# Kernel optimization log

Measured on AMD Instinct MI355X. Metric: run time of the kernel, lower is better.

Reference implementation:

```python
import jax, jax.numpy as jnp
import numpy as np

N_NODES = 30000
N_EDGES = 480000
NODE_DIM = 16
NUM_RADIAL = 8
NUM_ELEMENTS = 120
R_MAX = 5.0
NUM_BLOCKS = 2
N_PATHS = 5  # h0*sh0->0e, h0*sh1->1o, h0*sh2->2e, h1.sh1->0e, h2.sh2->0e


def _sh_basis(u):
    # real spherical harmonics up to l=2, component normalization, on unit vectors u [E,3]
    x, y, z = u[:, 0], u[:, 1], u[:, 2]
    s15 = jnp.sqrt(jnp.asarray(15.0, u.dtype))
    s5 = jnp.sqrt(jnp.asarray(5.0, u.dtype))
    sh1 = jnp.sqrt(jnp.asarray(3.0, u.dtype)) * u                      # [E,3]
    sh2 = jnp.stack([s15 * x * y, s15 * y * z,
                     0.5 * s5 * (3.0 * z * z - 1.0),
                     s15 * x * z, 0.5 * s15 * (x * x - y * y)], -1)    # [E,5]
    return sh1, sh2


def _energy(pos, emb, W_init, Wr, br, W_out, W_read, W1, b1, W2, b2, z, edge_index):
    N = pos.shape[0]
    row, col = edge_index[0], edge_index[1]
    edge_vec = pos[row] - pos[col]                                     # [E,3] gather
    r = jnp.sqrt(jnp.sum(edge_vec * edge_vec, -1) + 1e-12)             # [E]
    n = jnp.arange(1, NUM_RADIAL + 1, dtype=pos.dtype)
    # Bessel radial basis: sqrt(2/rc) * sin(n*pi*r/rc)/r
    radial = jnp.sqrt(2.0 / R_MAX) * jnp.sin(n[None, :] * jnp.pi * r[:, None] / R_MAX) / r[:, None]  # [E,R]
    u = edge_vec / r[:, None]
    sh1, sh2 = _sh_basis(u)

    # initial projection: embedding scalars -> 0e channels; l=1,l=2 start at zero
    h0 = emb[z] @ W_init                                               # [N,C]
    h1 = jnp.zeros((N, NODE_DIM, 3), pos.dtype)
    h2 = jnp.zeros((N, NODE_DIM, 5), pos.dtype)

    for b in range(NUM_BLOCKS):
        w = (radial @ Wr[b] + br[b]).reshape(-1, N_PATHS, NODE_DIM)    # [E,P,C] radial path weights
        h0c, h1c, h2c = h0[col], h1[col], h2[col]
        # scalar messages: h0*sh0 + <h1,sh1> + <h2,sh2>
        m0 = (w[:, 0] * h0c
              + w[:, 3] * jnp.einsum('ecm,em->ec', h1c, sh1)
              + w[:, 4] * jnp.einsum('ecm,em->ec', h2c, sh2))          # [E,C]
        m1 = (w[:, 1] * h0c)[:, :, None] * sh1[:, None, :]             # [E,C,3]
        m2 = (w[:, 2] * h0c)[:, :, None] * sh2[:, None, :]             # [E,C,5]
        a0 = jax.ops.segment_sum(m0, row, num_segments=N)
        a1 = jax.ops.segment_sum(m1, row, num_segments=N)
        a2 = jax.ops.segment_sum(m2, row, num_segments=N)
        h0 = h0 + a0 @ W_out[b, 0]
        h1 = h1 + jnp.einsum('ncm,cd->ndm', a1, W_out[b, 1])
        h2 = h2 + jnp.einsum('ncm,cd->ndm', a2, W_out[b, 2])

    inv = h0 @ W_read                                                  # readout 0e part
    site = jax.nn.silu(inv @ W1 + b1) @ W2 + b2                        # [N,1]
    return jnp.sum(site)


def setup_inputs() -> dict:
    key = jax.random.key(0)
    ks = jax.random.split(key, 12)
    C, R = NODE_DIM, NUM_RADIAL
    s = 1.0 / np.sqrt(C)
    return {
        'pos': jax.random.normal(ks[0], (N_NODES, 3), jnp.float32) * 3.0,
        'z': jax.random.randint(ks[1], (N_NODES,), 0, NUM_ELEMENTS),
        'edge_index': jax.random.randint(ks[2], (2, N_EDGES), 0, N_NODES),
        'emb': jax.random.normal(ks[3], (NUM_ELEMENTS, C), jnp.float32),
        'W_init': jax.random.normal(ks[4], (C, C), jnp.float32) * s,
        'Wr': jax.random.normal(ks[5], (NUM_BLOCKS, R, N_PATHS * C), jnp.float32) / np.sqrt(R),
        'br': jnp.zeros((NUM_BLOCKS, N_PATHS * C), jnp.float32),
        'W_out': jax.random.normal(ks[6], (NUM_BLOCKS, 3, C, C), jnp.float32) * s,
        'W_read': jax.random.normal(ks[7], (C, C), jnp.float32) * s,
        'W1': jax.random.normal(ks[8], (C, C), jnp.float32) * s,
        'b1': jnp.zeros((C,), jnp.float32),
        'W2': jax.random.normal(ks[9], (C, 1), jnp.float32) * s,
        'b2': jnp.zeros((1,), jnp.float32),
    }


def reference(pos, z, edge_index, emb, W_init, Wr, br, W_out, W_read, W1, b1, W2, b2):
    e_fn = lambda p: _energy(p, emb, W_init, Wr, br, W_out, W_read, W1, b1, W2, b2, z, edge_index)
    total, dE_dpos = jax.value_and_grad(e_fn)(pos)
    energy = jnp.reshape(total, (1, 1))
    forces = -dE_dpos
    return energy, forces
```

## Files before the change

kernel.cpp:

```cpp
#include <hip/hip_runtime.h>
#include <math.h>

#ifndef M_PI
#define M_PI 3.14159265358979323846
#endif

static inline int cdiv(int a, int b){ return (a + b - 1) / b; }

#define SQRT3f  1.7320508075688772f
#define SQRT5f  2.23606797749979f
#define SQRT15f 3.872983346207417f
#define KRADf   0.6324555320336759f
#define PI5f    0.6283185307179586f

__device__ __forceinline__ float grp16_sum(float v){
  v += __shfl_xor(v, 1, 64);
  v += __shfl_xor(v, 2, 64);
  v += __shfl_xor(v, 4, 64);
  v += __shfl_xor(v, 8, 64);
  return v;
}
__device__ __forceinline__ float xgrp_sum(float v){
  v += __shfl_xor(v, 16, 64);
  v += __shfl_xor(v, 32, 64);
  return v;
}

__device__ __forceinline__ void sh_from_u(float ux, float uy, float uz,
                                          float* sh1, float* sh2)
{
  sh1[0] = SQRT3f*ux; sh1[1] = SQRT3f*uy; sh1[2] = SQRT3f*uz;
  sh2[0] = SQRT15f*ux*uy;
  sh2[1] = SQRT15f*uy*uz;
  sh2[2] = 0.5f*SQRT5f*(3.f*uz*uz - 1.f);
  sh2[3] = SQRT15f*ux*uz;
  sh2[4] = 0.5f*SQRT15f*(ux*ux - uy*uy);
}

__global__ void k_hist(const int* __restrict__ ei, int E,
                       int* __restrict__ deg_row, int* __restrict__ deg_col)
{
  int e = blockIdx.x * blockDim.x + threadIdx.x;
  if (e >= E) return;
  atomicAdd(&deg_row[ei[e]], 1);
  atomicAdd(&deg_col[ei[E + e]], 1);
}

__global__ void k_alloc(const int* __restrict__ deg_row, const int* __restrict__ deg_col,
                        int* __restrict__ start_row, int* __restrict__ cur_row,
                        int* __restrict__ start_col, int* __restrict__ cur_col,
                        int* __restrict__ cursors, int N)
{
  int idx = blockIdx.x * blockDim.x + threadIdx.x;
  int lane = threadIdx.x & 63;
  #pragma unroll
  for (int which = 0; which < 2; which++) {
    const int* deg = which ? deg_col : deg_row;
    int* start = which ? start_col : start_row;
    int* cur   = which ? cur_col   : cur_row;
    int v = (idx < N) ? deg[idx] : 0;
    int incl = v;
    #pragma unroll
    for (int d = 1; d < 64; d <<= 1) {
      int y = __shfl_up(incl, d, 64);
      if (lane >= d) incl += y;
    }
    int wtot = __shfl(incl, 63, 64);
    int base = 0;
    if (lane == 63) base = atomicAdd(&cursors[which], wtot);
    base = __shfl(base, 63, 64);
    if (idx < N) { int st = base + incl - v; start[idx] = st; cur[idx] = st; }
  }
}

__global__ void k_scatter_geom(const float* __restrict__ pos, const int* __restrict__ ei, int E,
                               int* __restrict__ cur_row, int* __restrict__ cur_col,
                               float4* __restrict__ geoR,
                               int* __restrict__ colR, int* __restrict__ cposR,
                               int* __restrict__ rowC, int* __restrict__ rposC)
{
  int e = blockIdx.x * blockDim.x + threadIdx.x;
  if (e >= E) return;
  int row = ei[e], col = ei[E + e];
  int pr = atomicAdd(&cur_row[row], 1);
  int pc = atomicAdd(&cur_col[col], 1);
  colR[pr] = col; cposR[pr] = pc;
  rowC[pc] = row; rposC[pc] = pr;

  float px = pos[row*3+0] - pos[col*3+0];
  float py = pos[row*3+1] - pos[col*3+1];
  float pz = pos[row*3+2] - pos[col*3+2];
  float r2 = px*px + py*py + pz*pz + 1e-12f;
  float r = sqrtf(r2);
  float inv_r = 1.0f / r;
  float ux = px*inv_r, uy = py*inv_r, uz = pz*inv_r;
  float x = r * PI5f;
  float s1, c1;
  sincosf(x, &s1, &c1);
  float tc = 2.f * c1;
  float sprev = 0.f, s = s1, cprev = 1.f, cc = c1;
  float Ki = KRADf * inv_r;
  float rad[8], draddr[8];
  const float KPI5 = KRADf * PI5f;
  #pragma unroll
  for (int k = 0; k < 8; k++) {
    rad[k] = Ki * s;
    draddr[k] = (KPI5 * (float)(k+1) * cc - rad[k]) * inv_r;
    float sn = tc*s - sprev; sprev = s; s = sn;
    float cn = tc*cc - cprev; cprev = cc; cc = cn;
  }
  geoR[pr*5+0] = make_float4(rad[0], rad[1], rad[2], rad[3]);
  geoR[pr*5+1] = make_float4(rad[4], rad[5], rad[6], rad[7]);
  geoR[pr*5+2] = make_float4(draddr[0], draddr[1], draddr[2], draddr[3]);
  geoR[pr*5+3] = make_float4(draddr[4], draddr[5], draddr[6], draddr[7]);
  geoR[pr*5+4] = make_float4(ux, uy, uz, inv_r);
}

__global__ void k_node_init(const float* __restrict__ emb, const int* __restrict__ z,
                            const float* __restrict__ W_init, float* __restrict__ h0, int N)
{
  __shared__ float sW[256];
  if (threadIdx.x < 256) sW[threadIdx.x] = W_init[threadIdx.x];
  __syncthreads();
  int n = blockIdx.x * blockDim.x + threadIdx.x;
  if (n >= N) return;
  const float* e = emb + z[n]*16;
  float ev[16];
  #pragma unroll
  for (int k = 0; k < 16; k++) ev[k] = e[k];
  #pragma unroll
  for (int c = 0; c < 16; c++) {
    float s = 0.f;
    #pragma unroll
    for (int k = 0; k < 16; k++) s += ev[k] * sW[k*16+c];
    h0[n*16+c] = s;
  }
}

__global__ void k_fwd_b0(const float* __restrict__ Wr, const float* __restrict__ br,
                         const float* __restrict__ h0_in, const float4* __restrict__ geoR,
                         const int* __restrict__ colR,
                         const int* __restrict__ start_row, const int* __restrict__ deg_row,
                         float* __restrict__ a0, float* __restrict__ a1, float* __restrict__ a2,
                         int N)
{
  int n = (blockIdx.x * blockDim.x + threadIdx.x) >> 6;
  int lane = threadIdx.x & 63;
  int g = lane >> 4, c = lane & 15;
  if (n >= N) return;
  float wr0[8], wr1[8], wr2[8];
  #pragma unroll
  for (int k = 0; k < 8; k++) {
    wr0[k] = Wr[k*80 + c];
    wr1[k] = Wr[k*80 + 16 + c];
    wr2[k] = Wr[k*80 + 32 + c];
  }
  float b0v = br[c], b1v = br[16 + c], b2v = br[32 + c];

  float acc0 = 0.f, acc1[3] = {0.f,0.f,0.f}, acc2[5] = {0.f,0.f,0.f,0.f,0.f};

  int i0 = start_row[n] + g, i1 = start_row[n] + deg_row[n];
  float4 G0n = {0,0,0,0}, G1n = {0,0,0,0}, G4n = {0,0,0,0};
  float h0n = 0.f;
  if (i0 < i1) {
    G0n = geoR[i0*5+0]; G1n = geoR[i0*5+1]; G4n = geoR[i0*5+4];
    h0n = h0_in[colR[i0]*16 + c];
  }
  for (int i = i0; i < i1; i += 4) {
    float4 G0 = G0n, G1 = G1n, G4 = G4n;
    float h0c = h0n;
    if (i+4 < i1) {
      G0n = geoR[(i+4)*5+0]; G1n = geoR[(i+4)*5+1]; G4n = geoR[(i+4)*5+4];
      h0n = h0_in[colR[i+4]*16 + c];
    }
    float rad[8] = {G0.x,G0.y,G0.z,G0.w,G1.x,G1.y,G1.z,G1.w};
    float sh1[3], sh2[5];
    sh_from_u(G4.x, G4.y, G4.z, sh1, sh2);
    float w0 = b0v, w1 = b1v, w2 = b2v;
    #pragma unroll
    for (int k = 0; k < 8; k++) {
      w0 += rad[k]*wr0[k]; w1 += rad[k]*wr1[k]; w2 += rad[k]*wr2[k];
    }
    acc0 += w0*h0c;
    float wh1 = w1*h0c, wh2 = w2*h0c;
    #pragma unroll
    for (int m = 0; m < 3; m++) acc1[m] += wh1*sh1[m];
    #pragma unroll
    for (int m = 0; m < 5; m++) acc2[m] += wh2*sh2[m];
  }
  acc0 = xgrp_sum(acc0);
  #pragma unroll
  for (int m = 0; m < 3; m++) acc1[m] = xgrp_sum(acc1[m]);
  #pragma unroll
  for (int m = 0; m < 5; m++) acc2[m] = xgrp_sum(acc2[m]);
  if (g == 0) {
    a0[n*16 + c] = acc0;
    #pragma unroll
    for (int m = 0; m < 3; m++) a1[n*48 + c*3 + m] = acc1[m];
    #pragma unroll
    for (int m = 0; m < 5; m++) a2[n*80 + c*5 + m] = acc2[m];
  }
}

__global__ void k_fwd_b1(const float* __restrict__ Wr, const float* __restrict__ br,
                         const float* __restrict__ h0_in, const float* __restrict__ h1_in,
                         const float* __restrict__ h2_in, const float4* __restrict__ geoR,
                         const int* __restrict__ colR,
                         const int* __restrict__ start_row, const int* __restrict__ deg_row,
                         float* __restrict__ a0, int N)
{
  int n = (blockIdx.x * blockDim.x + threadIdx.x) >> 6;
  int lane = threadIdx.x & 63;
  int g = lane >> 4, c = lane & 15;
  if (n >= N) return;
  float wr0[8], wr3[8], wr4[8];
  #pragma unroll
  for (int k = 0; k < 8; k++) {
    wr0[k] = Wr[k*80 + c];
    wr3[k] = Wr[k*80 + 48 + c];
    wr4[k] = Wr[k*80 + 64 + c];
  }
  float b0v = br[c], b3v = br[48 + c], b4v = br[64 + c];

  float acc0 = 0.f;
  int i0 = start_row[n] + g, i1 = start_row[n] + deg_row[n];
  float4 G0n = {0,0,0,0}, G1n = {0,0,0,0}, G4n = {0,0,0,0};
  float h0n = 0.f, h1n[3] = {0,0,0}, h2n[5] = {0,0,0,0,0};
  if (i0 < i1) {
    int col = colR[i0];
    G0n = geoR[i0*5+0]; G1n = geoR[i0*5+1]; G4n = geoR[i0*5+4];
    h0n = h0_in[col*16 + c];
    #pragma unroll
    for (int m = 0; m < 3; m++) h1n[m] = h1_in[col*48 + c*3 + m];
    #pragma unroll
    for (int m = 0; m < 5; m++) h2n[m] = h2_in[col*80 + c*5 + m];
  }
  for (int i = i0; i < i1; i += 4) {
    float4 G0 = G0n, G1 = G1n, G4 = G4n;
    float h0c = h0n;
    float h1c[3], h2c[5];
    #pragma unroll
    for (int m = 0; m < 3; m++) h1c[m] = h1n[m];
    #pragma unroll
    for (int m = 0; m < 5; m++) h2c[m] = h2n[m];
    if (i+4 < i1) {
      int col = colR[i+4];
      G0n = geoR[(i+4)*5+0]; G1n = geoR[(i+4)*5+1]; G4n = geoR[(i+4)*5+4];
      h0n = h0_in[col*16 + c];
      #pragma unroll
      for (int m = 0; m < 3; m++) h1n[m] = h1_in[col*48 + c*3 + m];
      #pragma unroll
      for (int m = 0; m < 5; m++) h2n[m] = h2_in[col*80 + c*5 + m];
    }
    float rad[8] = {G0.x,G0.y,G0.z,G0.w,G1.x,G1.y,G1.z,G1.w};
    float sh1[3], sh2[5];
    sh_from_u(G4.x, G4.y, G4.z, sh1, sh2);
    float w0 = b0v, w3 = b3v, w4 = b4v;
    #pragma unroll
    for (int k = 0; k < 8; k++) {
      w0 += rad[k]*wr0[k]; w3 += rad[k]*wr3[k]; w4 += rad[k]*wr4[k];
    }
    float S1 = 0.f, S2 = 0.f;
    #pragma unroll
    for (int m = 0; m < 3; m++) S1 += h1c[m]*sh1[m];
    #pragma unroll
    for (int m = 0; m < 5; m++) S2 += h2c[m]*sh2[m];
    acc0 += w0*h0c + w3*S1 + w4*S2;
  }
  acc0 = xgrp_sum(acc0);
  if (g == 0) a0[n*16 + c] = acc0;
}

__global__ void k_node_update(const float* __restrict__ h0_in,
                              const float* __restrict__ a0, const float* __restrict__ a1,
                              const float* __restrict__ a2,
                              const float* __restrict__ U,
                              float* __restrict__ h0_out, float* __restrict__ h1_out,
                              float* __restrict__ h2_out, int N, int full)
{
  int idx = blockIdx.x * blockDim.x + threadIdx.x;
  int n = idx >> 4, d = idx & 15;
  if (n >= N) return;
  const float* U0 = U;
  const float* U1 = U + 256;
  const float* U2 = U + 512;
  float s = h0_in[n*16 + d];
  #pragma unroll
  for (int c = 0; c < 16; c++) s += a0[n*16 + c] * U0[c*16 + d];
  h0_out[n*16 + d] = s;
  if (full) {
    float v1[3] = {0.f, 0.f, 0.f};
    #pragma unroll
    for (int c = 0; c < 16; c++) {
      float u = U1[c*16 + d];
      #pragma unroll
      for (int m = 0; m < 3; m++) v1[m] += a1[n*48 + c*3 + m] * u;
    }
    #pragma unroll
    for (int m = 0; m < 3; m++) h1_out[n*48 + d*3 + m] = v1[m];
    float v2[5] = {0.f, 0.f, 0.f, 0.f, 0.f};
    #pragma unroll
    for (int c = 0; c < 16; c++) {
      float u = U2[c*16 + d];
      #pragma unroll
      for (int m = 0; m < 5; m++) v2[m] += a2[n*80 + c*5 + m] * u;
    }
    #pragma unroll
    for (int m = 0; m < 5; m++) h2_out[n*80 + d*5 + m] = v2[m];
  }
}

__global__ void k_readout_bwd(const float* __restrict__ h0, const float* __restrict__ W_read,
                              const float* __restrict__ W1, const float* __restrict__ b1,
                              const float* __restrict__ W2, const float* __restrict__ b2,
                              const float* __restrict__ U0b1,
                              float* __restrict__ g0, float* __restrict__ ga0,
                              float* __restrict__ energy, int N)
{
  int n = blockIdx.x * blockDim.x + threadIdx.x;
  float site = 0.f;
  if (n < N) {
    float h[16], inv[16], dt[16], g0v[16];
    #pragma unroll
    for (int d = 0; d < 16; d++) h[d] = h0[n*16 + d];
    #pragma unroll
    for (int j = 0; j < 16; j++) {
      float s = 0.f;
      #pragma unroll
      for (int d = 0; d < 16; d++) s += h[d] * W_read[d*16 + j];
      inv[j] = s;
    }
    site = b2[0];
    #pragma unroll
    for (int c = 0; c < 16; c++) {
      float t = b1[c];
      #pragma unroll
      for (int j = 0; j < 16; j++) t += inv[j] * W1[j*16 + c];
      float sg = 1.f / (1.f + expf(-t));
      float w2v = W2[c];
      site += t * sg * w2v;
      dt[c] = w2v * sg * (1.f + t * (1.f - sg));
    }
    float dinv[16];
    #pragma unroll
    for (int j = 0; j < 16; j++) {
      float s = 0.f;
      #pragma unroll
      for (int c = 0; c < 16; c++) s += dt[c] * W1[j*16 + c];
      dinv[j] = s;
    }
    #pragma unroll
    for (int d = 0; d < 16; d++) {
      float s = 0.f;
      #pragma unroll
      for (int j = 0; j < 16; j++) s += dinv[j] * W_read[d*16 + j];
      g0v[d] = s;
      g0[n*16 + d] = s;
    }
    #pragma unroll
    for (int c = 0; c < 16; c++) {
      float s = 0.f;
      #pragma unroll
      for (int d = 0; d < 16; d++) s += g0v[d] * U0b1[c*16 + d];
      ga0[n*16 + c] = s;
    }
  }
  #pragma unroll
  for (int off = 32; off; off >>= 1) site += __shfl_down(site, off, 64);
  if ((threadIdx.x & 63) == 0) atomicAdd(energy, site);
}

__global__ void k_ga(const float* __restrict__ g0, const float* __restrict__ g1,
                     const float* __restrict__ g2, const float* __restrict__ U,
                     float* __restrict__ ga0, float* __restrict__ ga1, float* __restrict__ ga2,
                     int N)
{
  int idx = blockIdx.x * blockDim.x + threadIdx.x;
  int n = idx >> 4, c = idx & 15;
  if (n >= N) return;
  const float* U0 = U;
  const float* U1 = U + 256;
  const float* U2 = U + 512;
  float s = 0.f;
  #pragma unroll
  for (int d = 0; d < 16; d++) s += g0[n*16 + d] * U0[c*16 + d];
  ga0[n*16 + c] = s;
  float v1[3] = {0.f, 0.f, 0.f};
  #pragma unroll
  for (int d = 0; d < 16; d++) {
    float u = U1[c*16 + d];
    #pragma unroll
    for (int m = 0; m < 3; m++) v1[m] += g1[n*48 + d*3 + m] * u;
  }
  #pragma unroll
  for (int m = 0; m < 3; m++) ga1[n*48 + c*3 + m] = v1[m];
  float v2[5] = {0.f, 0.f, 0.f, 0.f, 0.f};
  #pragma unroll
  for (int d = 0; d < 16; d++) {
    float u = U2[c*16 + d];
    #pragma unroll
    for (int m = 0; m < 5; m++) v2[m] += g2[n*80 + d*5 + m] * u;
  }
  #pragma unroll
  for (int m = 0; m < 5; m++) ga2[n*80 + c*5 + m] = v2[m];
}

__global__ void k_bwd_b1_col(const float* __restrict__ Wr, const float* __restrict__ br,
                             const float* __restrict__ h0_in, const float* __restrict__ h1_in,
                             const float* __restrict__ h2_in,
                             const float* __restrict__ ga0, const float4* __restrict__ geoR,
                             const int* __restrict__ rowC, const int* __restrict__ rposC,
                             const int* __restrict__ start_col, const int* __restrict__ deg_col,
                             float* __restrict__ g0, float* __restrict__ g1, float* __restrict__ g2,
                             float* __restrict__ dv_col, int N)
{
  int n = (blockIdx.x * blockDim.x + threadIdx.x) >> 6;
  int lane = threadIdx.x & 63;
  int g = lane >> 4, c = lane & 15;
  if (n >= N) return;
  float wr0[8], wr3[8], wr4[8];
  #pragma unroll
  for (int k = 0; k < 8; k++) {
    wr0[k] = Wr[k*80 + c];
    wr3[k] = Wr[k*80 + 48 + c];
    wr4[k] = Wr[k*80 + 64 + c];
  }
  float b0v = br[c], b3v = br[48 + c], b4v = br[64 + c];

  float h0c = h0_in[n*16 + c];
  float h1c[3], h2c[5];
  #pragma unroll
  for (int m = 0; m < 3; m++) h1c[m] = h1_in[n*48 + c*3 + m];
  #pragma unroll
  for (int m = 0; m < 5; m++) h2c[m] = h2_in[n*80 + c*5 + m];

  float accg0 = 0.f, accg1[3] = {0.f,0.f,0.f}, accg2[5] = {0.f,0.f,0.f,0.f,0.f};

  int i0 = start_col[n] + g, i1 = start_col[n] + deg_col[n];
  float4 G0n = {0,0,0,0}, G1n = {0,0,0,0}, G2n = {0,0,0,0}, G3n = {0,0,0,0}, G4n = {0,0,0,0};
  float dm0n = 0.f;
  if (i0 < i1) {
    int rp = rposC[i0];
    G0n = geoR[rp*5+0]; G1n = geoR[rp*5+1]; G2n = geoR[rp*5+2];
    G3n = geoR[rp*5+3]; G4n = geoR[rp*5+4];
    dm0n = ga0[rowC[i0]*16 + c];
  }
  for (int i = i0; i < i1; i += 4) {
    float4 G0 = G0n, G1 = G1n, G2 = G2n, G3 = G3n, G4 = G4n;
    float dm0 = dm0n;
    if (i+4 < i1) {
      int rp = rposC[i+4];
      G0n = geoR[rp*5+0]; G1n = geoR[rp*5+1]; G2n = geoR[rp*5+2];
      G3n = geoR[rp*5+3]; G4n = geoR[rp*5+4];
      dm0n = ga0[rowC[i+4]*16 + c];
    }
    float rad[8]    = {G0.x,G0.y,G0.z,G0.w,G1.x,G1.y,G1.z,G1.w};
    float draddr[8] = {G2.x,G2.y,G2.z,G2.w,G3.x,G3.y,G3.z,G3.w};
    float ux = G4.x, uy = G4.y, uz = G4.z, inv_r = G4.w;
    float sh1[3], sh2[5];
    sh_from_u(ux, uy, uz, sh1, sh2);

    float w0 = b0v, w3 = b3v, w4 = b4v;
    #pragma unroll
    for (int k = 0; k < 8; k++) {
      w0 += rad[k]*wr0[k]; w3 += rad[k]*wr3[k]; w4 += rad[k]*wr4[k];
    }

    float S1 = 0.f, S2 = 0.f;
    #pragma unroll
    for (int m = 0; m < 3; m++) S1 += h1c[m]*sh1[m];
    #pragma unroll
    for (int m = 0; m < 5; m++) S2 += h2c[m]*sh2[m];

    float dw0 = dm0 * h0c;
    float dw3 = dm0 * S1;
    float dw4 = dm0 * S2;
    float t3 = dm0 * w3, t4 = dm0 * w4;

    accg0 += dm0 * w0;
    #pragma unroll
    for (int m = 0; m < 3; m++) accg1[m] += t3 * sh1[m];
    #pragma unroll
    for (int m = 0; m < 5; m++) accg2[m] += t4 * sh2[m];

    float q1x = t3*h1c[0], q1y = t3*h1c[1], q1z = t3*h1c[2];
    float q0 = t4*h2c[0], q1 = t4*h2c[1], q2 = t4*h2c[2], q3 = t4*h2c[3], q4 = t4*h2c[4];
    float gr = 0.f;
    #pragma unroll
    for (int k = 0; k < 8; k++)
      gr += (dw0*wr0[k] + dw3*wr3[k] + dw4*wr4[k]) * draddr[k];
    float gux = SQRT3f*q1x + SQRT15f*(uy*q0 + uz*q3 + ux*q4);
    float guy = SQRT3f*q1y + SQRT15f*(ux*q0 + uz*q1 - uy*q4);
    float guz = SQRT3f*q1z + SQRT15f*uy*q1 + 3.f*SQRT5f*uz*q2 + SQRT15f*ux*q3;

    gr  = grp16_sum(gr);
    gux = grp16_sum(gux);
    guy = grp16_sum(guy);
    guz = grp16_sum(guz);

    if (c == 0) {
      float gdotu = gux*ux + guy*uy + guz*uz;
      dv_col[i*3+0] = gr*ux + (gux - gdotu*ux)*inv_r;
      dv_col[i*3+1] = gr*uy + (guy - gdotu*uy)*inv_r;
      dv_col[i*3+2] = gr*uz + (guz - gdotu*uz)*inv_r;
    }
  }
  accg0 = xgrp_sum(accg0);
  #pragma unroll
  for (int m = 0; m < 3; m++) accg1[m] = xgrp_sum(accg1[m]);
  #pragma unroll
  for (int m = 0; m < 5; m++) accg2[m] = xgrp_sum(accg2[m]);
  if (g == 0) {
    g0[n*16 + c] += accg0;
    #pragma unroll
    for (int m = 0; m < 3; m++) g1[n*48 + c*3 + m] = accg1[m];
    #pragma unroll
    for (int m = 0; m < 5; m++) g2[n*80 + c*5 + m] = accg2[m];
  }
}

__global__ void k_bwd_b0_row(const float* __restrict__ Wr, const float* __restrict__ br,
                             const float* __restrict__ h0_in,
                             const float* __restrict__ ga0, const float* __restrict__ ga1,
                             const float* __restrict__ ga2, const float4* __restrict__ geoR,
                             const int* __restrict__ colR, const int* __restrict__ cposR,
                             const int* __restrict__ start_row, const int* __restrict__ deg_row,
                             float* __restrict__ dv_col, int N)
{
  int n = (blockIdx.x * blockDim.x + threadIdx.x) >> 6;
  int lane = threadIdx.x & 63;
  int g = lane >> 4, c = lane & 15;
  if (n >= N) return;
  float wr0[8], wr1[8], wr2[8];
  #pragma unroll
  for (int k = 0; k < 8; k++) {
    wr0[k] = Wr[k*80 + c];
    wr1[k] = Wr[k*80 + 16 + c];
    wr2[k] = Wr[k*80 + 32 + c];
  }
  float b1v = br[16 + c], b2v = br[32 + c];

  float dm0 = ga0[n*16 + c];
  float dm1[3], dm2[5];
  #pragma unroll
  for (int m = 0; m < 3; m++) dm1[m] = ga1[n*48 + c*3 + m];
  #pragma unroll
  for (int m = 0; m < 5; m++) dm2[m] = ga2[n*80 + c*5 + m];

  int i0 = start_row[n] + g, i1 = start_row[n] + deg_row[n];
  float4 G0n = {0,0,0,0}, G1n = {0,0,0,0}, G2n = {0,0,0,0}, G3n = {0,0,0,0}, G4n = {0,0,0,0};
  float h0n = 0.f;
  if (i0 < i1) {
    G0n = geoR[i0*5+0]; G1n = geoR[i0*5+1]; G2n = geoR[i0*5+2];
    G3n = geoR[i0*5+3]; G4n = geoR[i0*5+4];
    h0n = h0_in[colR[i0]*16 + c];
  }
  for (int i = i0; i < i1; i += 4) {
    float4 G0 = G0n, G1 = G1n, G2 = G2n, G3 = G3n, G4 = G4n;
    float h0c = h0n;
    if (i+4 < i1) {
      G0n = geoR[(i+4)*5+0]; G1n = geoR[(i+4)*5+1]; G2n = geoR[(i+4)*5+2];
      G3n = geoR[(i+4)*5+3]; G4n = geoR[(i+4)*5+4];
      h0n = h0_in[colR[i+4]*16 + c];
    }
    float rad[8]    = {G0.x,G0.y,G0.z,G0.w,G1.x,G1.y,G1.z,G1.w};
    float draddr[8] = {G2.x,G2.y,G2.z,G2.w,G3.x,G3.y,G3.z,G3.w};
    float ux = G4.x, uy = G4.y, uz = G4.z, inv_r = G4.w;
    float sh1[3], sh2[5];
    sh_from_u(ux, uy, uz, sh1, sh2);

    float w1 = b1v, w2v = b2v;
    #pragma unroll
    for (int k = 0; k < 8; k++) { w1 += rad[k]*wr1[k]; w2v += rad[k]*wr2[k]; }

    float T1 = 0.f, T2 = 0.f;
    #pragma unroll
    for (int m = 0; m < 3; m++) T1 += dm1[m]*sh1[m];
    #pragma unroll
    for (int m = 0; m < 5; m++) T2 += dm2[m]*sh2[m];

    float dw0 = dm0 * h0c;
    float dw1 = h0c * T1;
    float dw2 = h0c * T2;

    float w1h = w1*h0c, w2h = w2v*h0c;
    float q1x = dm1[0]*w1h, q1y = dm1[1]*w1h, q1z = dm1[2]*w1h;
    float q0 = dm2[0]*w2h, q1 = dm2[1]*w2h, q2 = dm2[2]*w2h, q3 = dm2[3]*w2h, q4 = dm2[4]*w2h;

    float gr = 0.f;
    #pragma unroll
    for (int k = 0; k < 8; k++)
      gr += (dw0*wr0[k] + dw1*wr1[k] + dw2*wr2[k]) * draddr[k];
    float gux = SQRT3f*q1x + SQRT15f*(uy*q0 + uz*q3 + ux*q4);
    float guy = SQRT3f*q1y + SQRT15f*(ux*q0 + uz*q1 - uy*q4);
    float guz = SQRT3f*q1z + SQRT15f*uy*q1 + 3.f*SQRT5f*uz*q2 + SQRT15f*ux*q3;

    gr  = grp16_sum(gr);
    gux = grp16_sum(gux);
    guy = grp16_sum(guy);
    guz = grp16_sum(guz);

    if (c == 0) {
      int cp = cposR[i];
      float gdotu = gux*ux + guy*uy + guz*uz;
      dv_col[cp*3+0] += gr*ux + (gux - gdotu*ux)*inv_r;
      dv_col[cp*3+1] += gr*uy + (guy - gdotu*uy)*inv_r;
      dv_col[cp*3+2] += gr*uz + (guz - gdotu*uz)*inv_r;
    }
  }
}

__global__ void k_force(const int* __restrict__ start_row, const int* __restrict__ deg_row,
                        const int* __restrict__ cposR,
                        const int* __restrict__ start_col, const int* __restrict__ deg_col,
                        const float* __restrict__ dv_col, float* __restrict__ force, int N)
{
  int n = blockIdx.x * blockDim.x + threadIdx.x;
  if (n >= N) return;
  float fx = 0.f, fy = 0.f, fz = 0.f;
  int c0 = start_col[n], c1 = c0 + deg_col[n];
  for (int i = c0; i < c1; i++) {
    fx += dv_col[i*3+0]; fy += dv_col[i*3+1]; fz += dv_col[i*3+2];
  }
  int r0 = start_row[n], r1 = r0 + deg_row[n];
  for (int i = r0; i < r1; i++) {
    int cp = cposR[i];
    fx -= dv_col[cp*3+0]; fy -= dv_col[cp*3+1]; fz -= dv_col[cp*3+2];
  }
  force[n*3+0] = fx; force[n*3+1] = fy; force[n*3+2] = fz;
}

extern "C" void kernel_launch(void* const* d_in, const int* in_sizes, int n_in,
                              void* d_out, int out_size, void* d_ws, size_t ws_size,
                              hipStream_t stream)
{
  const float* pos    = (const float*)d_in[0];
  const int*   z      = (const int*)  d_in[1];
  const int*   ei     = (const int*)  d_in[2];
  const float* emb    = (const float*)d_in[3];
  const float* W_init = (const float*)d_in[4];
  const float* Wr     = (const float*)d_in[5];
  const float* br     = (const float*)d_in[6];
  const float* W_out  = (const float*)d_in[7];
  const float* W_read = (const float*)d_in[8];
  const float* W1     = (const float*)d_in[9];
  const float* b1     = (const float*)d_in[10];
  const float* W2     = (const float*)d_in[11];
  const float* b2     = (const float*)d_in[12];

  const int N = in_sizes[0] / 3;
  const int E = in_sizes[2] / 2;

  float* f = (float*)d_ws;
  float* geo_f = f; f += (size_t)E*20;
  float* h0_s0 = f; f += (size_t)N*16;
  float* h0_s1 = f; f += (size_t)N*16;
  float* h0_s2 = f; f += (size_t)N*16;
  float* h1_s1 = f; f += (size_t)N*48;
  float* h2_s1 = f; f += (size_t)N*80;
  float* a0    = f; f += (size_t)N*16;
  float* a1    = f; f += (size_t)N*48;
  float* a2    = f; f += (size_t)N*80;
  float* g0    = f; f += (size_t)N*16;
  float* g1    = f; f += (size_t)N*48;
  float* g2    = f; f += (size_t)N*80;
  float* dv    = f; f += (size_t)E*3;
  int* ip = (int*)f;
  int* cursors   = ip; ip += 2;
  int* deg_row   = ip; ip += N;
  int* deg_col   = ip; ip += N;
  int* start_row = ip; ip += N;
  int* start_col = ip; ip += N;
  int* cur_row   = ip; ip += N;
  int* cur_col   = ip; ip += N;
  int* colR      = ip; ip += E;
  int* cposR     = ip; ip += E;
  int* rowC      = ip; ip += E;
  int* rposC     = ip; ip += E;

  float4* geoR = (float4*)geo_f;

  float* out    = (float*)d_out;
  float* energy = out;
  float* force  = out + 1;

  const int BLK = 256;
  const int NPB = BLK / 64;
  const int GPB = BLK / 16;

  (void)hipMemsetAsync(energy, 0, sizeof(float), stream);
  (void)hipMemsetAsync(cursors, 0, (size_t)(2 + 2*N) * sizeof(int), stream);

  k_hist<<<cdiv(E, BLK), BLK, 0, stream>>>(ei, E, deg_row, deg_col);
  k_alloc<<<cdiv(N, BLK), BLK, 0, stream>>>(deg_row, deg_col, start_row, cur_row,
                                            start_col, cur_col, cursors, N);
  k_scatter_geom<<<cdiv(E, BLK), BLK, 0, stream>>>(pos, ei, E, cur_row, cur_col,
                                                   geoR, colR, cposR, rowC, rposC);

  k_node_init<<<cdiv(N, BLK), BLK, 0, stream>>>(emb, z, W_init, h0_s0, N);

  k_fwd_b0<<<cdiv(N, NPB), BLK, 0, stream>>>(Wr, br, h0_s0, geoR, colR,
                                             start_row, deg_row, a0, a1, a2, N);
  k_node_update<<<cdiv(N*16, BLK), BLK, 0, stream>>>(h0_s0, a0, a1, a2,
                                                     W_out, h0_s1, h1_s1, h2_s1, N, 1);

  k_fwd_b1<<<cdiv(N, NPB), BLK, 0, stream>>>(Wr + 640, br + 80,
                                             h0_s1, h1_s1, h2_s1, geoR, colR,
                                             start_row, deg_row, a0, N);
  k_node_update<<<cdiv(N*16, BLK), BLK, 0, stream>>>(h0_s1, a0, nullptr, nullptr,
                                                     W_out + 768, h0_s2, nullptr, nullptr, N, 0);

  k_readout_bwd<<<cdiv(N, BLK), BLK, 0, stream>>>(h0_s2, W_read, W1, b1, W2, b2,
                                                  W_out + 768, g0, a0, energy, N);

  k_bwd_b1_col<<<cdiv(N, NPB), BLK, 0, stream>>>(Wr + 640, br + 80,
                                                 h0_s1, h1_s1, h2_s1, a0, geoR,
                                                 rowC, rposC, start_col, deg_col,
                                                 g0, g1, g2, dv, N);

  k_ga<<<cdiv(N*16, BLK), BLK, 0, stream>>>(g0, g1, g2, W_out, a0, a1, a2, N);
  k_bwd_b0_row<<<cdiv(N, NPB), BLK, 0, stream>>>(Wr, br, h0_s0,
                                                 a0, a1, a2, geoR, colR, cposR,
                                                 start_row, deg_row, dv, N);

  k_force<<<cdiv(N, BLK), BLK, 0, stream>>>(start_row, deg_row, cposR,
                                            start_col, deg_col, dv, force, N);
}
```

Measured before the change: 529.3 us.

## Store compact edge geometry in row and col order, recompute radial basis on the fly

Replaces the 80-byte per-edge geometry record (radial, radial derivative, unit vector) with a 16-byte unit vector plus an 8-byte sin/cos pair, duplicated in row-sorted and col-sorted order. Each edge kernel now rebuilds the Bessel radial values and their derivatives from sin/cos with the Chebyshev recurrence. The col-ordered backward kernel reads contiguous data instead of gathering through rposC. The row backward kernel writes its own dv buffer directly, removing a read-modify-write via cposR, and the force kernel combines both buffers. This trades memory traffic and indirect gathers for a little extra ALU work and one extra E*3 buffer.

```diff
diff --git a/kernel.cpp b/kernel.cpp
--- a/kernel.cpp
+++ b/kernel.cpp
@@ -37,6 +37,33 @@
   sh2[4] = 0.5f*SQRT15f*(ux*ux - uy*uy);
 }
 
+__device__ __forceinline__ void rad_from_sc(float s1, float c1, float inv_r, float* rad)
+{
+  float tc = 2.f * c1;
+  float sprev = 0.f, s = s1;
+  float Ki = KRADf * inv_r;
+  #pragma unroll
+  for (int k = 0; k < 8; k++) {
+    rad[k] = Ki * s;
+    float sn = tc*s - sprev; sprev = s; s = sn;
+  }
+}
+__device__ __forceinline__ void rad_drad_from_sc(float s1, float c1, float inv_r,
+                                                 float* rad, float* draddr)
+{
+  float tc = 2.f * c1;
+  float sprev = 0.f, s = s1, cprev = 1.f, cc = c1;
+  float Ki = KRADf * inv_r;
+  const float KPI5 = KRADf * PI5f;
+  #pragma unroll
+  for (int k = 0; k < 8; k++) {
+    rad[k] = Ki * s;
+    draddr[k] = (KPI5 * (float)(k+1) * cc - rad[k]) * inv_r;
+    float sn = tc*s - sprev; sprev = s; s = sn;
+    float cn = tc*cc - cprev; cprev = cc; cc = cn;
+  }
+}
+
 __global__ void k_hist(const int* __restrict__ ei, int E,
                        int* __restrict__ deg_row, int* __restrict__ deg_col)
 {
@@ -75,7 +102,8 @@
 
 __global__ void k_scatter_geom(const float* __restrict__ pos, const int* __restrict__ ei, int E,
                                int* __restrict__ cur_row, int* __restrict__ cur_col,
-                               float4* __restrict__ geoR,
+                               float4* __restrict__ uR, float2* __restrict__ scR,
+                               float4* __restrict__ uC, float2* __restrict__ scC,
                                int* __restrict__ colR, int* __restrict__ cposR,
                                int* __restrict__ rowC, int* __restrict__ rposC)
 {
@@ -94,26 +122,12 @@
   float r = sqrtf(r2);
   float inv_r = 1.0f / r;
   float ux = px*inv_r, uy = py*inv_r, uz = pz*inv_r;
-  float x = r * PI5f;
   float s1, c1;
-  sincosf(x, &s1, &c1);
-  float tc = 2.f * c1;
-  float sprev = 0.f, s = s1, cprev = 1.f, cc = c1;
-  float Ki = KRADf * inv_r;
-  float rad[8], draddr[8];
-  const float KPI5 = KRADf * PI5f;
-  #pragma unroll
-  for (int k = 0; k < 8; k++) {
-    rad[k] = Ki * s;
-    draddr[k] = (KPI5 * (float)(k+1) * cc - rad[k]) * inv_r;
-    float sn = tc*s - sprev; sprev = s; s = sn;
-    float cn = tc*cc - cprev; cprev = cc; cc = cn;
-  }
-  geoR[pr*5+0] = make_float4(rad[0], rad[1], rad[2], rad[3]);
-  geoR[pr*5+1] = make_float4(rad[4], rad[5], rad[6], rad[7]);
-  geoR[pr*5+2] = make_float4(draddr[0], draddr[1], draddr[2], draddr[3]);
-  geoR[pr*5+3] = make_float4(draddr[4], draddr[5], draddr[6], draddr[7]);
-  geoR[pr*5+4] = make_float4(ux, uy, uz, inv_r);
+  sincosf(r * PI5f, &s1, &c1);
+  float4 u4 = make_float4(ux, uy, uz, inv_r);
+  float2 sc = make_float2(s1, c1);
+  uR[pr] = u4; scR[pr] = sc;
+  uC[pc] = u4; scC[pc] = sc;
 }
 
 __global__ void k_node_init(const float* __restrict__ emb, const int* __restrict__ z,
@@ -138,7 +152,8 @@
 }
 
 __global__ void k_fwd_b0(const float* __restrict__ Wr, const float* __restrict__ br,
-                         const float* __restrict__ h0_in, const float4* __restrict__ geoR,
+                         const float* __restrict__ h0_in,
+                         const float4* __restrict__ uR, const float2* __restrict__ scR,
                          const int* __restrict__ colR,
                          const int* __restrict__ start_row, const int* __restrict__ deg_row,
                          float* __restrict__ a0, float* __restrict__ a1, float* __restrict__ a2,
@@ -160,22 +175,23 @@
   float acc0 = 0.f, acc1[3] = {0.f,0.f,0.f}, acc2[5] = {0.f,0.f,0.f,0.f,0.f};
 
   int i0 = start_row[n] + g, i1 = start_row[n] + deg_row[n];
-  float4 G0n = {0,0,0,0}, G1n = {0,0,0,0}, G4n = {0,0,0,0};
+  float4 Un = {0,0,0,0}; float2 SCn = {0,0};
   float h0n = 0.f;
   if (i0 < i1) {
-    G0n = geoR[i0*5+0]; G1n = geoR[i0*5+1]; G4n = geoR[i0*5+4];
+    Un = uR[i0]; SCn = scR[i0];
     h0n = h0_in[colR[i0]*16 + c];
   }
   for (int i = i0; i < i1; i += 4) {
-    float4 G0 = G0n, G1 = G1n, G4 = G4n;
+    float4 U = Un; float2 SC = SCn;
     float h0c = h0n;
     if (i+4 < i1) {
-      G0n = geoR[(i+4)*5+0]; G1n = geoR[(i+4)*5+1]; G4n = geoR[(i+4)*5+4];
+      Un = uR[i+4]; SCn = scR[i+4];
       h0n = h0_in[colR[i+4]*16 + c];
     }
-    float rad[8] = {G0.x,G0.y,G0.z,G0.w,G1.x,G1.y,G1.z,G1.w};
+    float rad[8];
+    rad_from_sc(SC.x, SC.y, U.w, rad);
     float sh1[3], sh2[5];
-    sh_from_u(G4.x, G4.y, G4.z, sh1, sh2);
+    sh_from_u(U.x, U.y, U.z, sh1, sh2);
     float w0 = b0v, w1 = b1v, w2 = b2v;
     #pragma unroll
     for (int k = 0; k < 8; k++) {
@@ -204,7 +220,8 @@
 
 __global__ void k_fwd_b1(const float* __restrict__ Wr, const float* __restrict__ br,
                          const float* __restrict__ h0_in, const float* __restrict__ h1_in,
-                         const float* __restrict__ h2_in, const float4* __restrict__ geoR,
+                         const float* __restrict__ h2_in,
+                         const float4* __restrict__ uR, const float2* __restrict__ scR,
                          const int* __restrict__ colR,
                          const int* __restrict__ start_row, const int* __restrict__ deg_row,
                          float* __restrict__ a0, int N)
@@ -224,11 +241,11 @@
 
   float acc0 = 0.f;
   int i0 = start_row[n] + g, i1 = start_row[n] + deg_row[n];
-  float4 G0n = {0,0,0,0}, G1n = {0,0,0,0}, G4n = {0,0,0,0};
+  float4 Un = {0,0,0,0}; float2 SCn = {0,0};
   float h0n = 0.f, h1n[3] = {0,0,0}, h2n[5] = {0,0,0,0,0};
   if (i0 < i1) {
     int col = colR[i0];
-    G0n = geoR[i0*5+0]; G1n = geoR[i0*5+1]; G4n = geoR[i0*5+4];
+    Un = uR[i0]; SCn = scR[i0];
     h0n = h0_in[col*16 + c];
     #pragma unroll
     for (int m = 0; m < 3; m++) h1n[m] = h1_in[col*48 + c*3 + m];
@@ -236,7 +253,7 @@
     for (int m = 0; m < 5; m++) h2n[m] = h2_in[col*80 + c*5 + m];
   }
   for (int i = i0; i < i1; i += 4) {
-    float4 G0 = G0n, G1 = G1n, G4 = G4n;
+    float4 U = Un; float2 SC = SCn;
     float h0c = h0n;
     float h1c[3], h2c[5];
     #pragma unroll
@@ -245,16 +262,17 @@
     for (int m = 0; m < 5; m++) h2c[m] = h2n[m];
     if (i+4 < i1) {
       int col = colR[i+4];
-      G0n = geoR[(i+4)*5+0]; G1n = geoR[(i+4)*5+1]; G4n = geoR[(i+4)*5+4];
+      Un = uR[i+4]; SCn = scR[i+4];
       h0n = h0_in[col*16 + c];
       #pragma unroll
       for (int m = 0; m < 3; m++) h1n[m] = h1_in[col*48 + c*3 + m];
       #pragma unroll
       for (int m = 0; m < 5; m++) h2n[m] = h2_in[col*80 + c*5 + m];
     }
-    float rad[8] = {G0.x,G0.y,G0.z,G0.w,G1.x,G1.y,G1.z,G1.w};
+    float rad[8];
+    rad_from_sc(SC.x, SC.y, U.w, rad);
     float sh1[3], sh2[5];
-    sh_from_u(G4.x, G4.y, G4.z, sh1, sh2);
+    sh_from_u(U.x, U.y, U.z, sh1, sh2);
     float w0 = b0v, w3 = b3v, w4 = b4v;
     #pragma unroll
     for (int k = 0; k < 8; k++) {
@@ -408,8 +426,9 @@
 __global__ void k_bwd_b1_col(const float* __restrict__ Wr, const float* __restrict__ br,
                              const float* __restrict__ h0_in, const float* __restrict__ h1_in,
                              const float* __restrict__ h2_in,
-                             const float* __restrict__ ga0, const float4* __restrict__ geoR,
-                             const int* __restrict__ rowC, const int* __restrict__ rposC,
+                             const float* __restrict__ ga0,
+                             const float4* __restrict__ uC, const float2* __restrict__ scC,
+                             const int* __restrict__ rowC,
                              const int* __restrict__ start_col, const int* __restrict__ deg_col,
                              float* __restrict__ g0, float* __restrict__ g1, float* __restrict__ g2,
                              float* __restrict__ dv_col, int N)
@@ -437,26 +456,22 @@
   float accg0 = 0.f, accg1[3] = {0.f,0.f,0.f}, accg2[5] = {0.f,0.f,0.f,0.f,0.f};
 
   int i0 = start_col[n] + g, i1 = start_col[n] + deg_col[n];
-  float4 G0n = {0,0,0,0}, G1n = {0,0,0,0}, G2n = {0,0,0,0}, G3n = {0,0,0,0}, G4n = {0,0,0,0};
+  float4 Un = {0,0,0,0}; float2 SCn = {0,0};
   float dm0n = 0.f;
   if (i0 < i1) {
-    int rp = rposC[i0];
-    G0n = geoR[rp*5+0]; G1n = geoR[rp*5+1]; G2n = geoR[rp*5+2];
-    G3n = geoR[rp*5+3]; G4n = geoR[rp*5+4];
+    Un = uC[i0]; SCn = scC[i0];
     dm0n = ga0[rowC[i0]*16 + c];
   }
   for (int i = i0; i < i1; i += 4) {
-    float4 G0 = G0n, G1 = G1n, G2 = G2n, G3 = G3n, G4 = G4n;
+    float4 U = Un; float2 SC = SCn;
     float dm0 = dm0n;
     if (i+4 < i1) {
-      int rp = rposC[i+4];
-      G0n = geoR[rp*5+0]; G1n = geoR[rp*5+1]; G2n = geoR[rp*5+2];
-      G3n = geoR[rp*5+3]; G4n = geoR[rp*5+4];
+      Un = uC[i+4]; SCn = scC[i+4];
       dm0n = ga0[rowC[i+4]*16 + c];
     }
-    float rad[8]    = {G0.x,G0.y,G0.z,G0.w,G1.x,G1.y,G1.z,G1.w};
-    float draddr[8] = {G2.x,G2.y,G2.z,G2.w,G3.x,G3.y,G3.z,G3.w};
-    float ux = G4.x, uy = G4.y, uz = G4.z, inv_r = G4.w;
+    float rad[8], draddr[8];
+    rad_drad_from_sc(SC.x, SC.y, U.w, rad, draddr);
+    float ux = U.x, uy = U.y, uz = U.z, inv_r = U.w;
     float sh1[3], sh2[5];
     sh_from_u(ux, uy, uz, sh1, sh2);
 
@@ -522,10 +537,11 @@
 __global__ void k_bwd_b0_row(const float* __restrict__ Wr, const float* __restrict__ br,
                              const float* __restrict__ h0_in,
                              const float* __restrict__ ga0, const float* __restrict__ ga1,
-                             const float* __restrict__ ga2, const float4* __restrict__ geoR,
-                             const int* __restrict__ colR, const int* __restrict__ cposR,
+                             const float* __restrict__ ga2,
+                             const float4* __restrict__ uR, const float2* __restrict__ scR,
+                             const int* __restrict__ colR,
                              const int* __restrict__ start_row, const int* __restrict__ deg_row,
-                             float* __restrict__ dv_col, int N)
+                             float* __restrict__ dv_row, int N)
 {
   int n = (blockIdx.x * blockDim.x + threadIdx.x) >> 6;
   int lane = threadIdx.x & 63;
@@ -548,24 +564,22 @@
   for (int m = 0; m < 5; m++) dm2[m] = ga2[n*80 + c*5 + m];
 
   int i0 = start_row[n] + g, i1 = start_row[n] + deg_row[n];
-  float4 G0n = {0,0,0,0}, G1n = {0,0,0,0}, G2n = {0,0,0,0}, G3n = {0,0,0,0}, G4n = {0,0,0,0};
+  float4 Un = {0,0,0,0}; float2 SCn = {0,0};
   float h0n = 0.f;
   if (i0 < i1) {
-    G0n = geoR[i0*5+0]; G1n = geoR[i0*5+1]; G2n = geoR[i0*5+2];
-    G3n = geoR[i0*5+3]; G4n = geoR[i0*5+4];
+    Un = uR[i0]; SCn = scR[i0];
     h0n = h0_in[colR[i0]*16 + c];
   }
   for (int i = i0; i < i1; i += 4) {
-    float4 G0 = G0n, G1 = G1n, G2 = G2n, G3 = G3n, G4 = G4n;
+    float4 U = Un; float2 SC = SCn;
     float h0c = h0n;
     if (i+4 < i1) {
-      G0n = geoR[(i+4)*5+0]; G1n = geoR[(i+4)*5+1]; G2n = geoR[(i+4)*5+2];
-      G3n = geoR[(i+4)*5+3]; G4n = geoR[(i+4)*5+4];
+      Un = uR[i+4]; SCn = scR[i+4];
       h0n = h0_in[colR[i+4]*16 + c];
     }
-    float rad[8]    = {G0.x,G0.y,G0.z,G0.w,G1.x,G1.y,G1.z,G1.w};
-    float draddr[8] = {G2.x,G2.y,G2.z,G2.w,G3.x,G3.y,G3.z,G3.w};
-    float ux = G4.x, uy = G4.y, uz = G4.z, inv_r = G4.w;
+    float rad[8], draddr[8];
+    rad_drad_from_sc(SC.x, SC.y, U.w, rad, draddr);
+    float ux = U.x, uy = U.y, uz = U.z, inv_r = U.w;
     float sh1[3], sh2[5];
     sh_from_u(ux, uy, uz, sh1, sh2);
 
@@ -601,11 +615,10 @@
     guz = grp16_sum(guz);
 
     if (c == 0) {
-      int cp = cposR[i];
       float gdotu = gux*ux + guy*uy + guz*uz;
-      dv_col[cp*3+0] += gr*ux + (gux - gdotu*ux)*inv_r;
-      dv_col[cp*3+1] += gr*uy + (guy - gdotu*uy)*inv_r;
-      dv_col[cp*3+2] += gr*uz + (guz - gdotu*uz)*inv_r;
+      dv_row[i*3+0] = gr*ux + (gux - gdotu*ux)*inv_r;
+      dv_row[i*3+1] = gr*uy + (guy - gdotu*uy)*inv_r;
+      dv_row[i*3+2] = gr*uz + (guz - gdotu*uz)*inv_r;
     }
   }
 }
@@ -613,19 +626,26 @@
 __global__ void k_force(const int* __restrict__ start_row, const int* __restrict__ deg_row,
                         const int* __restrict__ cposR,
                         const int* __restrict__ start_col, const int* __restrict__ deg_col,
-                        const float* __restrict__ dv_col, float* __restrict__ force, int N)
+                        const int* __restrict__ rposC,
+                        const float* __restrict__ dv_col, const float* __restrict__ dv_row,
+                        float* __restrict__ force, int N)
 {
   int n = blockIdx.x * blockDim.x + threadIdx.x;
   if (n >= N) return;
   float fx = 0.f, fy = 0.f, fz = 0.f;
   int c0 = start_col[n], c1 = c0 + deg_col[n];
   for (int i = c0; i < c1; i++) {
-    fx += dv_col[i*3+0]; fy += dv_col[i*3+1]; fz += dv_col[i*3+2];
+    int rp = rposC[i];
+    fx += dv_col[i*3+0] + dv_row[rp*3+0];
+    fy += dv_col[i*3+1] + dv_row[rp*3+1];
+    fz += dv_col[i*3+2] + dv_row[rp*3+2];
   }
   int r0 = start_row[n], r1 = r0 + deg_row[n];
   for (int i = r0; i < r1; i++) {
     int cp = cposR[i];
-    fx -= dv_col[cp*3+0]; fy -= dv_col[cp*3+1]; fz -= dv_col[cp*3+2];
+    fx -= dv_row[i*3+0] + dv_col[cp*3+0];
+    fy -= dv_row[i*3+1] + dv_col[cp*3+1];
+    fz -= dv_row[i*3+2] + dv_col[cp*3+2];
   }
   force[n*3+0] = fx; force[n*3+1] = fy; force[n*3+2] = fz;
 }
@@ -652,7 +672,10 @@
   const int E = in_sizes[2] / 2;
 
   float* f = (float*)d_ws;
-  float* geo_f = f; f += (size_t)E*20;
+  float4* uR  = (float4*)f; f += (size_t)E*4;
+  float4* uC  = (float4*)f; f += (size_t)E*4;
+  float2* scR = (float2*)f; f += (size_t)E*2;
+  float2* scC = (float2*)f; f += (size_t)E*2;
   float* h0_s0 = f; f += (size_t)N*16;
   float* h0_s1 = f; f += (size_t)N*16;
   float* h0_s2 = f; f += (size_t)N*16;
@@ -664,7 +687,8 @@
   float* g0    = f; f += (size_t)N*16;
   float* g1    = f; f += (size_t)N*48;
   float* g2    = f; f += (size_t)N*80;
-  float* dv    = f; f += (size_t)E*3;
+  float* dv_c  = f; f += (size_t)E*3;
+  float* dv_r  = f; f += (size_t)E*3;
   int* ip = (int*)f;
   int* cursors   = ip; ip += 2;
   int* deg_row   = ip; ip += N;
@@ -678,15 +702,12 @@
   int* rowC      = ip; ip += E;
   int* rposC     = ip; ip += E;
 
-  float4* geoR = (float4*)geo_f;
-
   float* out    = (float*)d_out;
   float* energy = out;
   float* force  = out + 1;
 
   const int BLK = 256;
   const int NPB = BLK / 64;
-  const int GPB = BLK / 16;
 
   (void)hipMemsetAsync(energy, 0, sizeof(float), stream);
   (void)hipMemsetAsync(cursors, 0, (size_t)(2 + 2*N) * sizeof(int), stream);
@@ -695,17 +716,18 @@
   k_alloc<<<cdiv(N, BLK), BLK, 0, stream>>>(deg_row, deg_col, start_row, cur_row,
                                             start_col, cur_col, cursors, N);
   k_scatter_geom<<<cdiv(E, BLK), BLK, 0, stream>>>(pos, ei, E, cur_row, cur_col,
-                                                   geoR, colR, cposR, rowC, rposC);
+                                                   uR, scR, uC, scC,
+                                                   colR, cposR, rowC, rposC);
 
   k_node_init<<<cdiv(N, BLK), BLK, 0, stream>>>(emb, z, W_init, h0_s0, N);
 
-  k_fwd_b0<<<cdiv(N, NPB), BLK, 0, stream>>>(Wr, br, h0_s0, geoR, colR,
+  k_fwd_b0<<<cdiv(N, NPB), BLK, 0, stream>>>(Wr, br, h0_s0, uR, scR, colR,
                                              start_row, deg_row, a0, a1, a2, N);
   k_node_update<<<cdiv(N*16, BLK), BLK, 0, stream>>>(h0_s0, a0, a1, a2,
                                                      W_out, h0_s1, h1_s1, h2_s1, N, 1);
 
   k_fwd_b1<<<cdiv(N, NPB), BLK, 0, stream>>>(Wr + 640, br + 80,
-                                             h0_s1, h1_s1, h2_s1, geoR, colR,
+                                             h0_s1, h1_s1, h2_s1, uR, scR, colR,
                                              start_row, deg_row, a0, N);
   k_node_update<<<cdiv(N*16, BLK), BLK, 0, stream>>>(h0_s1, a0, nullptr, nullptr,
                                                      W_out + 768, h0_s2, nullptr, nullptr, N, 0);
@@ -714,15 +736,16 @@
                                                   W_out + 768, g0, a0, energy, N);
 
   k_bwd_b1_col<<<cdiv(N, NPB), BLK, 0, stream>>>(Wr + 640, br + 80,
-                                                 h0_s1, h1_s1, h2_s1, a0, geoR,
-                                                 rowC, rposC, start_col, deg_col,
-                                                 g0, g1, g2, dv, N);
+                                                 h0_s1, h1_s1, h2_s1, a0,
+                                                 uC, scC, rowC, start_col, deg_col,
+                                                 g0, g1, g2, dv_c, N);
 
   k_ga<<<cdiv(N*16, BLK), BLK, 0, stream>>>(g0, g1, g2, W_out, a0, a1, a2, N);
   k_bwd_b0_row<<<cdiv(N, NPB), BLK, 0, stream>>>(Wr, br, h0_s0,
-                                                 a0, a1, a2, geoR, colR, cposR,
-                                                 start_row, deg_row, dv, N);
+                                                 a0, a1, a2, uR, scR, colR,
+                                                 start_row, deg_row, dv_r, N);
 
   k_force<<<cdiv(N, BLK), BLK, 0, stream>>>(start_row, deg_row, cposR,
-                                            start_col, deg_col, dv, force, N);
-}
+                                            start_col, deg_col, rposC,
+                                            dv_c, dv_r, force, N);
+}
```

After: 514.2 us. -2.9%, faster.
